# Performance work log

Hardware: AMD Instinct MI355X
Metric: run time of the kernel (lower is better)

Reference implementation:

```python
import jax, jax.numpy as jnp
import numpy as np

N, NUM_CLASSES, FEAT_DIM = 32768, 395, 512


def setup_inputs() -> dict:
    key = jax.random.key(0)
    k1, k2, k3, k4 = jax.random.split(key, 4)
    modal1_inputs = jax.random.normal(k1, (N, FEAT_DIM), dtype=jnp.float32)
    modal2_inputs = jax.random.normal(k2, (N, FEAT_DIM), dtype=jnp.float32)
    targets = jax.random.randint(k3, (N,), 0, NUM_CLASSES)
    # learned centers parameter: torch.rand -> uniform [0, 1)
    centers = jax.random.uniform(k4, (NUM_CLASSES, FEAT_DIM), dtype=jnp.float32)
    return {
        "modal1_inputs": modal1_inputs,
        "modal2_inputs": modal2_inputs,
        "centers": centers,
        "targets": targets,
    }


def _smooth_l1(a, b):
    # SmoothL1Loss with default beta=1.0, reduction='mean'
    d = jnp.abs(a - b)
    return jnp.mean(jnp.where(d < 1.0, 0.5 * d * d, d - 0.5))


def reference(modal1_inputs, modal2_inputs, centers, targets):
    num_classes = centers.shape[0]
    # Per-label mean (the original O(N^2) loop is exactly a segment mean
    # gathered back per sample).
    ones = jnp.ones((targets.shape[0],), dtype=modal1_inputs.dtype)
    counts = jax.ops.segment_sum(ones, targets, num_segments=num_classes)
    counts = jnp.maximum(counts, 1.0)  # empty classes never gathered
    sum1 = jax.ops.segment_sum(modal1_inputs, targets, num_segments=num_classes)
    sum2 = jax.ops.segment_sum(modal2_inputs, targets, num_segments=num_classes)
    centersR = (sum1 / counts[:, None])[targets]  # [N, D]
    centersT = (sum2 / counts[:, None])[targets]  # [N, D]
    gathered_centers = centers[targets]           # [N, D]
    loss = _smooth_l1(centersR, gathered_centers) + _smooth_l1(centersT, gathered_centers)
    return loss
```

## Files before the change

### kernel.cpp

```cpp
#include <hip/hip_runtime.h>

#define NS 32768
#define NC 395
#define FD 512
#define SPL 8
#define CHUNK (NS / SPL)
#define TPB 256
#define NEL (NC * FD)

__device__ float g_partial[SPL * 2 * NC * FD];
__device__ int   g_pcount[SPL * NC];

__device__ __forceinline__ void f4add(float4& a, const float4 b) {
    a.x += b.x; a.y += b.y; a.z += b.z; a.w += b.w;
}

__global__ __launch_bounds__(TPB)
void gather_sum_kernel(const float4* __restrict__ m1,
                       const float4* __restrict__ m2,
                       const int* __restrict__ targets,
                       float* __restrict__ out) {
    int c   = blockIdx.x >> 3;
    int s   = blockIdx.x & (SPL - 1);
    int tid = threadIdx.x;

    if (blockIdx.x == 0 && tid == 0) out[0] = 0.0f;

    __shared__ int sidx[CHUNK];
    __shared__ int scnt;
    __shared__ float4 cmb[2][128];

    int sbase = s * CHUNK;
    const int4* t4 = reinterpret_cast<const int4*>(targets + sbase);
    int4 ta = t4[tid];
    int4 tb = t4[tid + TPB];
    int4 tc = t4[tid + 2 * TPB];
    int4 td = t4[tid + 3 * TPB];
    if (tid == 0) scnt = 0;
    __syncthreads();
    int i0 = sbase + 4 * tid;
    int i1 = sbase + 4 * (tid + TPB);
    int i2 = sbase + 4 * (tid + 2 * TPB);
    int i3 = sbase + 4 * (tid + 3 * TPB);
    if (ta.x == c) sidx[atomicAdd(&scnt, 1)] = i0;
    if (ta.y == c) sidx[atomicAdd(&scnt, 1)] = i0 + 1;
    if (ta.z == c) sidx[atomicAdd(&scnt, 1)] = i0 + 2;
    if (ta.w == c) sidx[atomicAdd(&scnt, 1)] = i0 + 3;
    if (tb.x == c) sidx[atomicAdd(&scnt, 1)] = i1;
    if (tb.y == c) sidx[atomicAdd(&scnt, 1)] = i1 + 1;
    if (tb.z == c) sidx[atomicAdd(&scnt, 1)] = i1 + 2;
    if (tb.w == c) sidx[atomicAdd(&scnt, 1)] = i1 + 3;
    if (tc.x == c) sidx[atomicAdd(&scnt, 1)] = i2;
    if (tc.y == c) sidx[atomicAdd(&scnt, 1)] = i2 + 1;
    if (tc.z == c) sidx[atomicAdd(&scnt, 1)] = i2 + 2;
    if (tc.w == c) sidx[atomicAdd(&scnt, 1)] = i2 + 3;
    if (td.x == c) sidx[atomicAdd(&scnt, 1)] = i3;
    if (td.y == c) sidx[atomicAdd(&scnt, 1)] = i3 + 1;
    if (td.z == c) sidx[atomicAdd(&scnt, 1)] = i3 + 2;
    if (td.w == c) sidx[atomicAdd(&scnt, 1)] = i3 + 3;
    __syncthreads();
    int cnt = scnt;

    int wid  = tid >> 6;
    int mod  = wid >> 1;
    int wsub = wid & 1;
    int lane = tid & 63;
    const float4* src = mod ? m2 : m1;

    float4 z = make_float4(0.f, 0.f, 0.f, 0.f);
    float4 aA0 = z, aB0 = z, aA1 = z, aB1 = z;

    int j = wsub;
    for (; j + 6 < cnt; j += 8) {
        const float4* p0 = src + (size_t)sidx[j]     * 128;
        const float4* p1 = src + (size_t)sidx[j + 2] * 128;
        const float4* p2 = src + (size_t)sidx[j + 4] * 128;
        const float4* p3 = src + (size_t)sidx[j + 6] * 128;
        float4 vA0 = p0[lane], vB0 = p0[lane + 64];
        float4 vA1 = p1[lane], vB1 = p1[lane + 64];
        float4 vA2 = p2[lane], vB2 = p2[lane + 64];
        float4 vA3 = p3[lane], vB3 = p3[lane + 64];
        f4add(aA0, vA0); f4add(aB0, vB0);
        f4add(aA1, vA1); f4add(aB1, vB1);
        f4add(aA0, vA2); f4add(aB0, vB2);
        f4add(aA1, vA3); f4add(aB1, vB3);
    }
    for (; j < cnt; j += 2) {
        const float4* p = src + (size_t)sidx[j] * 128;
        f4add(aA0, p[lane]); f4add(aB0, p[lane + 64]);
    }
    f4add(aA0, aA1); f4add(aB0, aB1);

    if (wsub == 0) {
        cmb[mod][lane]      = aA0;
        cmb[mod][lane + 64] = aB0;
    }
    __syncthreads();
    if (wsub == 1) {
        float4 rA = cmb[mod][lane];      f4add(rA, aA0);
        float4 rB = cmb[mod][lane + 64]; f4add(rB, aB0);
        float4* dst = reinterpret_cast<float4*>(g_partial);
        size_t base = (((size_t)s * 2 + mod) * NC + c) * 128;
        dst[base + lane]      = rA;
        dst[base + lane + 64] = rB;
    }
    if (tid == 0) g_pcount[s * NC + c] = cnt;
}

__device__ __forceinline__ float smooth_l1(float d) {
    d = fabsf(d);
    return d < 1.0f ? 0.5f * d * d : d - 0.5f;
}

__global__ void loss_kernel(const float* __restrict__ centers,
                            float* __restrict__ out) {
    __shared__ float scnt[NC];
    int t = threadIdx.x;
    for (int c = t; c < NC; c += 256) {
        int sc = 0;
        #pragma unroll
        for (int k = 0; k < SPL; k++) sc += g_pcount[k * NC + c];
        scnt[c] = (float)sc;
    }
    __syncthreads();

    float val = 0.0f;
    for (int gid = blockIdx.x * 256 + t; gid < NEL; gid += gridDim.x * 256) {
        int c = gid >> 9;
        float cnt = scnt[c];
        if (cnt > 0.0f) {
            float s1 = 0.0f, s2 = 0.0f;
            #pragma unroll
            for (int k = 0; k < SPL; k++) {
                s1 += g_partial[(size_t)(2 * k)     * NEL + gid];
                s2 += g_partial[(size_t)(2 * k + 1) * NEL + gid];
            }
            float ctr = centers[gid];
            float inv = 1.0f / cnt;
            val += cnt * (smooth_l1(s1 * inv - ctr) + smooth_l1(s2 * inv - ctr));
        }
    }

    for (int off = 32; off > 0; off >>= 1)
        val += __shfl_down(val, off, 64);
    __shared__ float wsum[4];
    int lane = t & 63, wid = t >> 6;
    if (lane == 0) wsum[wid] = val;
    __syncthreads();
    if (t == 0) {
        float sm = wsum[0] + wsum[1] + wsum[2] + wsum[3];
        atomicAdd(out, sm * 5.9604644775390625e-08f);
    }
}

extern "C" void kernel_launch(void* const* d_in, const int* in_sizes, int n_in,
                              void* d_out, int out_size, void* d_ws, size_t ws_size,
                              hipStream_t stream) {
    const float4* m1 = (const float4*)d_in[0];
    const float4* m2 = (const float4*)d_in[1];
    const float* centers = (const float*)d_in[2];
    const int* targets = (const int*)d_in[3];
    float* out = (float*)d_out;

    gather_sum_kernel<<<NC * SPL, TPB, 0, stream>>>(m1, m2, targets, out);
    loss_kernel<<<512, 256, 0, stream>>>(centers, out);
}
```

Baseline: 168.5 us.

## Replace per-block target scanning with global counting sort of sample indices

Before, every one of the class×split blocks re-read its whole chunk of the targets array and filtered it with shared-memory atomics. Now a histogram, a prefix scan and a scatter kernel build a sorted index list once. Each class's range in that list is split into 4 quarters per gather block, which replaces the 8 chunk splits. This removes the redundant target scanning and halves the partial buffer the loss kernel reads, at the cost of three extra small launches including a single-block prefix kernel.

```diff
diff --git a/kernel.cpp b/kernel.cpp
--- a/kernel.cpp
+++ b/kernel.cpp
@@ -3,79 +3,99 @@
 #define NS 32768
 #define NC 395
 #define FD 512
-#define SPL 8
-#define CHUNK (NS / SPL)
-#define TPB 256
 #define NEL (NC * FD)
 
-__device__ float g_partial[SPL * 2 * NC * FD];
-__device__ int   g_pcount[SPL * NC];
+#define HBLK 64
+#define QPC 4
+
+__device__ int   g_histp[HBLK * NC];
+__device__ int   g_off[NC + 1];
+__device__ int   g_cur[NC];
+__device__ int   g_sorted[NS];
+__device__ float g_part[QPC * 2 * NC * FD];
+
+__global__ __launch_bounds__(256)
+void k_hist(const int* __restrict__ targets) {
+    __shared__ int h[NC];
+    int t = threadIdx.x;
+    for (int c = t; c < NC; c += 256) h[c] = 0;
+    __syncthreads();
+    int base = blockIdx.x * 512;
+    atomicAdd(&h[targets[base + t]], 1);
+    atomicAdd(&h[targets[base + t + 256]], 1);
+    __syncthreads();
+    for (int c = t; c < NC; c += 256) g_histp[blockIdx.x * NC + c] = h[c];
+}
+
+__global__ __launch_bounds__(512)
+void k_prefix(float* __restrict__ out) {
+    __shared__ int sh[512];
+    int t = threadIdx.x;
+    int v = 0;
+    if (t < NC)
+        for (int b = 0; b < HBLK; b++) v += g_histp[b * NC + t];
+    sh[t] = v;
+    __syncthreads();
+    for (int off = 1; off < 512; off <<= 1) {
+        int x = sh[t];
+        if (t >= off) x += sh[t - off];
+        __syncthreads();
+        sh[t] = x;
+        __syncthreads();
+    }
+    if (t < NC) {
+        int excl = sh[t] - v;
+        g_off[t] = excl;
+        g_cur[t] = excl;
+    }
+    if (t == NC - 1) g_off[NC] = sh[t];
+    if (t == 0) out[0] = 0.0f;
+}
+
+__global__ __launch_bounds__(256)
+void k_scatter(const int* __restrict__ targets) {
+    int i = blockIdx.x * 256 + threadIdx.x;
+    int c = targets[i];
+    int pos = atomicAdd(&g_cur[c], 1);
+    g_sorted[pos] = i;
+}
 
 __device__ __forceinline__ void f4add(float4& a, const float4 b) {
     a.x += b.x; a.y += b.y; a.z += b.z; a.w += b.w;
 }
 
-__global__ __launch_bounds__(TPB)
-void gather_sum_kernel(const float4* __restrict__ m1,
-                       const float4* __restrict__ m2,
-                       const int* __restrict__ targets,
-                       float* __restrict__ out) {
-    int c   = blockIdx.x >> 3;
-    int s   = blockIdx.x & (SPL - 1);
+__global__ __launch_bounds__(256)
+void k_gather(const float4* __restrict__ m1, const float4* __restrict__ m2) {
+    int c   = blockIdx.x >> 2;
+    int q   = blockIdx.x & (QPC - 1);
     int tid = threadIdx.x;
 
-    if (blockIdx.x == 0 && tid == 0) out[0] = 0.0f;
-
-    __shared__ int sidx[CHUNK];
-    __shared__ int scnt;
-    __shared__ float4 cmb[2][128];
-
-    int sbase = s * CHUNK;
-    const int4* t4 = reinterpret_cast<const int4*>(targets + sbase);
-    int4 ta = t4[tid];
-    int4 tb = t4[tid + TPB];
-    int4 tc = t4[tid + 2 * TPB];
-    int4 td = t4[tid + 3 * TPB];
-    if (tid == 0) scnt = 0;
-    __syncthreads();
-    int i0 = sbase + 4 * tid;
-    int i1 = sbase + 4 * (tid + TPB);
-    int i2 = sbase + 4 * (tid + 2 * TPB);
-    int i3 = sbase + 4 * (tid + 3 * TPB);
-    if (ta.x == c) sidx[atomicAdd(&scnt, 1)] = i0;
-    if (ta.y == c) sidx[atomicAdd(&scnt, 1)] = i0 + 1;
-    if (ta.z == c) sidx[atomicAdd(&scnt, 1)] = i0 + 2;
-    if (ta.w == c) sidx[atomicAdd(&scnt, 1)] = i0 + 3;
-    if (tb.x == c) sidx[atomicAdd(&scnt, 1)] = i1;
-    if (tb.y == c) sidx[atomicAdd(&scnt, 1)] = i1 + 1;
-    if (tb.z == c) sidx[atomicAdd(&scnt, 1)] = i1 + 2;
-    if (tb.w == c) sidx[atomicAdd(&scnt, 1)] = i1 + 3;
-    if (tc.x == c) sidx[atomicAdd(&scnt, 1)] = i2;
-    if (tc.y == c) sidx[atomicAdd(&scnt, 1)] = i2 + 1;
-    if (tc.z == c) sidx[atomicAdd(&scnt, 1)] = i2 + 2;
-    if (tc.w == c) sidx[atomicAdd(&scnt, 1)] = i2 + 3;
-    if (td.x == c) sidx[atomicAdd(&scnt, 1)] = i3;
-    if (td.y == c) sidx[atomicAdd(&scnt, 1)] = i3 + 1;
-    if (td.z == c) sidx[atomicAdd(&scnt, 1)] = i3 + 2;
-    if (td.w == c) sidx[atomicAdd(&scnt, 1)] = i3 + 3;
-    __syncthreads();
-    int cnt = scnt;
+    int o0 = g_off[c], o1 = g_off[c + 1];
+    int n  = o1 - o0;
+    int s0 = o0 + ((n * q) >> 2);
+    int s1 = o0 + ((n * (q + 1)) >> 2);
 
     int wid  = tid >> 6;
     int mod  = wid >> 1;
-    int wsub = wid & 1;
+    int par  = wid & 1;
     int lane = tid & 63;
     const float4* src = mod ? m2 : m1;
 
     float4 z = make_float4(0.f, 0.f, 0.f, 0.f);
     float4 aA0 = z, aB0 = z, aA1 = z, aB1 = z;
 
-    int j = wsub;
-    for (; j + 6 < cnt; j += 8) {
-        const float4* p0 = src + (size_t)sidx[j]     * 128;
-        const float4* p1 = src + (size_t)sidx[j + 2] * 128;
-        const float4* p2 = src + (size_t)sidx[j + 4] * 128;
-        const float4* p3 = src + (size_t)sidx[j + 6] * 128;
+    __shared__ float4 cmb[2][128];
+
+    int j = s0 + par;
+    for (; j + 6 < s1; j += 8) {
+        int i0 = g_sorted[j];
+        int i1 = g_sorted[j + 2];
+        int i2 = g_sorted[j + 4];
+        int i3 = g_sorted[j + 6];
+        const float4* p0 = src + (size_t)i0 * 128;
+        const float4* p1 = src + (size_t)i1 * 128;
+        const float4* p2 = src + (size_t)i2 * 128;
+        const float4* p3 = src + (size_t)i3 * 128;
         float4 vA0 = p0[lane], vB0 = p0[lane + 64];
         float4 vA1 = p1[lane], vB1 = p1[lane + 64];
         float4 vA2 = p2[lane], vB2 = p2[lane + 64];
@@ -85,26 +105,25 @@
         f4add(aA0, vA2); f4add(aB0, vB2);
         f4add(aA1, vA3); f4add(aB1, vB3);
     }
-    for (; j < cnt; j += 2) {
-        const float4* p = src + (size_t)sidx[j] * 128;
+    for (; j < s1; j += 2) {
+        const float4* p = src + (size_t)g_sorted[j] * 128;
         f4add(aA0, p[lane]); f4add(aB0, p[lane + 64]);
     }
     f4add(aA0, aA1); f4add(aB0, aB1);
 
-    if (wsub == 0) {
+    if (par == 0) {
         cmb[mod][lane]      = aA0;
         cmb[mod][lane + 64] = aB0;
     }
     __syncthreads();
-    if (wsub == 1) {
+    if (par == 1) {
         float4 rA = cmb[mod][lane];      f4add(rA, aA0);
         float4 rB = cmb[mod][lane + 64]; f4add(rB, aB0);
-        float4* dst = reinterpret_cast<float4*>(g_partial);
-        size_t base = (((size_t)s * 2 + mod) * NC + c) * 128;
+        float4* dst = reinterpret_cast<float4*>(g_part);
+        size_t base = (((size_t)q * 2 + mod) * NC + c) * 128;
         dst[base + lane]      = rA;
         dst[base + lane + 64] = rB;
     }
-    if (tid == 0) g_pcount[s * NC + c] = cnt;
 }
 
 __device__ __forceinline__ float smooth_l1(float d) {
@@ -112,16 +131,12 @@
     return d < 1.0f ? 0.5f * d * d : d - 0.5f;
 }
 
-__global__ void loss_kernel(const float* __restrict__ centers,
-                            float* __restrict__ out) {
+__global__ void k_loss(const float* __restrict__ centers,
+                       float* __restrict__ out) {
     __shared__ float scnt[NC];
     int t = threadIdx.x;
-    for (int c = t; c < NC; c += 256) {
-        int sc = 0;
-        #pragma unroll
-        for (int k = 0; k < SPL; k++) sc += g_pcount[k * NC + c];
-        scnt[c] = (float)sc;
-    }
+    for (int c = t; c < NC; c += 256)
+        scnt[c] = (float)(g_off[c + 1] - g_off[c]);
     __syncthreads();
 
     float val = 0.0f;
@@ -131,9 +146,9 @@
         if (cnt > 0.0f) {
             float s1 = 0.0f, s2 = 0.0f;
             #pragma unroll
-            for (int k = 0; k < SPL; k++) {
-                s1 += g_partial[(size_t)(2 * k)     * NEL + gid];
-                s2 += g_partial[(size_t)(2 * k + 1) * NEL + gid];
+            for (int k = 0; k < QPC; k++) {
+                s1 += g_part[(size_t)(2 * k)     * NEL + gid];
+                s2 += g_part[(size_t)(2 * k + 1) * NEL + gid];
             }
             float ctr = centers[gid];
             float inv = 1.0f / cnt;
@@ -162,6 +177,9 @@
     const int* targets = (const int*)d_in[3];
     float* out = (float*)d_out;
 
-    gather_sum_kernel<<<NC * SPL, TPB, 0, stream>>>(m1, m2, targets, out);
-    loss_kernel<<<512, 256, 0, stream>>>(centers, out);
+    k_hist<<<NS / 512, 256, 0, stream>>>(targets);
+    k_prefix<<<1, 512, 0, stream>>>(out);
+    k_scatter<<<NS / 256, 256, 0, stream>>>(targets);
+    k_gather<<<NC * QPC, 256, 0, stream>>>(m1, m2);
+    k_loss<<<512, 256, 0, stream>>>(centers, out);
 }
```

Result: slower. 184.3 us (+9.3%).

## Replace per-class gather with streaming row pass and shared-memory atomic accumulation

Applied to the files above, without the earlier changes.

The segment sum is restructured. Each block used to scan the targets for one class and gather matching rows. Now each block streams a contiguous row range for one 32-float column slice and accumulates into a per-class table in LDS with shared atomics. Inputs are read once, fully coalesced, with prefetching, which removes the repeated target scans and scattered row gathers. The cost is heavy LDS atomic traffic, only 512 blocks, and a larger partial buffer (16 splits) that the loss kernel must now reduce, which it does with float4 loads.

```diff
diff --git a/kernel.cpp b/kernel.cpp
--- a/kernel.cpp
+++ b/kernel.cpp
@@ -3,108 +3,102 @@
 #define NS 32768
 #define NC 395
 #define FD 512
-#define SPL 8
-#define CHUNK (NS / SPL)
-#define TPB 256
 #define NEL (NC * FD)
 
-__device__ float g_partial[SPL * 2 * NC * FD];
-__device__ int   g_pcount[SPL * NC];
+#define RS 16
+#define CT 16
+#define TF4 8
+#define ROWS_PB (NS / RS)
+#define ASTRIDE 33
+
+__device__ float g_part[2 * RS * NC * FD];
+__device__ int   g_hist[RS * NC];
 
 __device__ __forceinline__ void f4add(float4& a, const float4 b) {
     a.x += b.x; a.y += b.y; a.z += b.z; a.w += b.w;
 }
 
-__global__ __launch_bounds__(TPB)
-void gather_sum_kernel(const float4* __restrict__ m1,
-                       const float4* __restrict__ m2,
-                       const int* __restrict__ targets,
-                       float* __restrict__ out) {
-    int c   = blockIdx.x >> 3;
-    int s   = blockIdx.x & (SPL - 1);
-    int tid = threadIdx.x;
+__global__ __launch_bounds__(256, 2)
+void k_stream(const float4* __restrict__ m1, const float4* __restrict__ m2,
+              const int* __restrict__ targets, float* __restrict__ out) {
+    int bid = blockIdx.x;
+    int ct  = bid & (CT - 1);
+    int mod = (bid >> 4) & 1;
+    int rs  = bid >> 5;
+    int t   = threadIdx.x;
 
-    if (blockIdx.x == 0 && tid == 0) out[0] = 0.0f;
+    __shared__ float acc[NC * ASTRIDE];
+    __shared__ int   tg[ROWS_PB];
 
-    __shared__ int sidx[CHUNK];
-    __shared__ int scnt;
-    __shared__ float4 cmb[2][128];
+    for (int i = t; i < NC * ASTRIDE; i += 256) acc[i] = 0.f;
 
-    int sbase = s * CHUNK;
-    const int4* t4 = reinterpret_cast<const int4*>(targets + sbase);
-    int4 ta = t4[tid];
-    int4 tb = t4[tid + TPB];
-    int4 tc = t4[tid + 2 * TPB];
-    int4 td = t4[tid + 3 * TPB];
-    if (tid == 0) scnt = 0;
+    const int4* t4 = reinterpret_cast<const int4*>(targets + rs * ROWS_PB);
+    reinterpret_cast<int4*>(tg)[t]       = t4[t];
+    reinterpret_cast<int4*>(tg)[t + 256] = t4[t + 256];
+    if (bid == 0 && t == 0) out[0] = 0.f;
     __syncthreads();
-    int i0 = sbase + 4 * tid;
-    int i1 = sbase + 4 * (tid + TPB);
-    int i2 = sbase + 4 * (tid + 2 * TPB);
-    int i3 = sbase + 4 * (tid + 3 * TPB);
-    if (ta.x == c) sidx[atomicAdd(&scnt, 1)] = i0;
-    if (ta.y == c) sidx[atomicAdd(&scnt, 1)] = i0 + 1;
-    if (ta.z == c) sidx[atomicAdd(&scnt, 1)] = i0 + 2;
-    if (ta.w == c) sidx[atomicAdd(&scnt, 1)] = i0 + 3;
-    if (tb.x == c) sidx[atomicAdd(&scnt, 1)] = i1;
-    if (tb.y == c) sidx[atomicAdd(&scnt, 1)] = i1 + 1;
-    if (tb.z == c) sidx[atomicAdd(&scnt, 1)] = i1 + 2;
-    if (tb.w == c) sidx[atomicAdd(&scnt, 1)] = i1 + 3;
-    if (tc.x == c) sidx[atomicAdd(&scnt, 1)] = i2;
-    if (tc.y == c) sidx[atomicAdd(&scnt, 1)] = i2 + 1;
-    if (tc.z == c) sidx[atomicAdd(&scnt, 1)] = i2 + 2;
-    if (tc.w == c) sidx[atomicAdd(&scnt, 1)] = i2 + 3;
-    if (td.x == c) sidx[atomicAdd(&scnt, 1)] = i3;
-    if (td.y == c) sidx[atomicAdd(&scnt, 1)] = i3 + 1;
-    if (td.z == c) sidx[atomicAdd(&scnt, 1)] = i3 + 2;
-    if (td.w == c) sidx[atomicAdd(&scnt, 1)] = i3 + 3;
+
+    const float4* src = mod ? m2 : m1;
+    int rsub = t >> 3;
+    int cf4  = t & 7;
+    const float4* sp = src + (size_t)rs * ROWS_PB * 128 + ct * TF4 + cf4;
+
+    float4 v0,v1,v2,v3,v4,v5,v6,v7;
+    v0 = sp[(size_t)(0*32 + rsub) * 128];
+    v1 = sp[(size_t)(1*32 + rsub) * 128];
+    v2 = sp[(size_t)(2*32 + rsub) * 128];
+    v3 = sp[(size_t)(3*32 + rsub) * 128];
+    v4 = sp[(size_t)(4*32 + rsub) * 128];
+    v5 = sp[(size_t)(5*32 + rsub) * 128];
+    v6 = sp[(size_t)(6*32 + rsub) * 128];
+    v7 = sp[(size_t)(7*32 + rsub) * 128];
+
+    #define ACCUM(U, V)                                                      \
+    {   int cls = tg[(rb + U) * 32 + rsub];                                  \
+        float* ap = &acc[cls * ASTRIDE + cf4 * 4];                           \
+        atomicAdd(ap + 0, V.x); atomicAdd(ap + 1, V.y);                      \
+        atomicAdd(ap + 2, V.z); atomicAdd(ap + 3, V.w); }
+
+    for (int rb = 0; rb < 56; rb += 8) {
+        float4 w0,w1,w2,w3,w4,w5,w6,w7;
+        w0 = sp[(size_t)((rb+ 8)*32 + rsub) * 128];
+        w1 = sp[(size_t)((rb+ 9)*32 + rsub) * 128];
+        w2 = sp[(size_t)((rb+10)*32 + rsub) * 128];
+        w3 = sp[(size_t)((rb+11)*32 + rsub) * 128];
+        w4 = sp[(size_t)((rb+12)*32 + rsub) * 128];
+        w5 = sp[(size_t)((rb+13)*32 + rsub) * 128];
+        w6 = sp[(size_t)((rb+14)*32 + rsub) * 128];
+        w7 = sp[(size_t)((rb+15)*32 + rsub) * 128];
+        ACCUM(0, v0) ACCUM(1, v1) ACCUM(2, v2) ACCUM(3, v3)
+        ACCUM(4, v4) ACCUM(5, v5) ACCUM(6, v6) ACCUM(7, v7)
+        v0=w0; v1=w1; v2=w2; v3=w3; v4=w4; v5=w5; v6=w6; v7=w7;
+    }
+    {
+        const int rb = 56;
+        ACCUM(0, v0) ACCUM(1, v1) ACCUM(2, v2) ACCUM(3, v3)
+        ACCUM(4, v4) ACCUM(5, v5) ACCUM(6, v6) ACCUM(7, v7)
+    }
+    #undef ACCUM
     __syncthreads();
-    int cnt = scnt;
 
-    int wid  = tid >> 6;
-    int mod  = wid >> 1;
-    int wsub = wid & 1;
-    int lane = tid & 63;
-    const float4* src = mod ? m2 : m1;
+    float4* dst = reinterpret_cast<float4*>(g_part)
+                + (size_t)(mod * RS + rs) * (NEL / 4) + ct * TF4;
+    for (int i = t; i < NC * TF4; i += 256) {
+        int cls = i >> 3, cf = i & 7;
+        const float* ap = &acc[cls * ASTRIDE + cf * 4];
+        float4 vv; vv.x = ap[0]; vv.y = ap[1]; vv.z = ap[2]; vv.w = ap[3];
+        dst[(size_t)cls * (FD / 4) + cf] = vv;
+    }
 
-    float4 z = make_float4(0.f, 0.f, 0.f, 0.f);
-    float4 aA0 = z, aB0 = z, aA1 = z, aB1 = z;
-
-    int j = wsub;
-    for (; j + 6 < cnt; j += 8) {
-        const float4* p0 = src + (size_t)sidx[j]     * 128;
-        const float4* p1 = src + (size_t)sidx[j + 2] * 128;
-        const float4* p2 = src + (size_t)sidx[j + 4] * 128;
-        const float4* p3 = src + (size_t)sidx[j + 6] * 128;
-        float4 vA0 = p0[lane], vB0 = p0[lane + 64];
-        float4 vA1 = p1[lane], vB1 = p1[lane + 64];
-        float4 vA2 = p2[lane], vB2 = p2[lane + 64];
-        float4 vA3 = p3[lane], vB3 = p3[lane + 64];
-        f4add(aA0, vA0); f4add(aB0, vB0);
-        f4add(aA1, vA1); f4add(aB1, vB1);
-        f4add(aA0, vA2); f4add(aB0, vB2);
-        f4add(aA1, vA3); f4add(aB1, vB3);
+    if (ct == 0 && mod == 0) {
+        __syncthreads();
+        int* h = reinterpret_cast<int*>(acc);
+        for (int i = t; i < NC; i += 256) h[i] = 0;
+        __syncthreads();
+        for (int i = t; i < ROWS_PB; i += 256) atomicAdd(&h[tg[i]], 1);
+        __syncthreads();
+        for (int i = t; i < NC; i += 256) g_hist[rs * NC + i] = h[i];
     }
-    for (; j < cnt; j += 2) {
-        const float4* p = src + (size_t)sidx[j] * 128;
-        f4add(aA0, p[lane]); f4add(aB0, p[lane + 64]);
-    }
-    f4add(aA0, aA1); f4add(aB0, aB1);
-
-    if (wsub == 0) {
-        cmb[mod][lane]      = aA0;
-        cmb[mod][lane + 64] = aB0;
-    }
-    __syncthreads();
-    if (wsub == 1) {
-        float4 rA = cmb[mod][lane];      f4add(rA, aA0);
-        float4 rB = cmb[mod][lane + 64]; f4add(rB, aB0);
-        float4* dst = reinterpret_cast<float4*>(g_partial);
-        size_t base = (((size_t)s * 2 + mod) * NC + c) * 128;
-        dst[base + lane]      = rA;
-        dst[base + lane + 64] = rB;
-    }
-    if (tid == 0) g_pcount[s * NC + c] = cnt;
 }
 
 __device__ __forceinline__ float smooth_l1(float d) {
@@ -112,32 +106,38 @@
     return d < 1.0f ? 0.5f * d * d : d - 0.5f;
 }
 
-__global__ void loss_kernel(const float* __restrict__ centers,
-                            float* __restrict__ out) {
+__global__ __launch_bounds__(256)
+void k_loss(const float* __restrict__ centers, float* __restrict__ out) {
     __shared__ float scnt[NC];
     int t = threadIdx.x;
     for (int c = t; c < NC; c += 256) {
-        int sc = 0;
+        int s = 0;
         #pragma unroll
-        for (int k = 0; k < SPL; k++) sc += g_pcount[k * NC + c];
-        scnt[c] = (float)sc;
+        for (int k = 0; k < RS; ++k) s += g_hist[k * NC + c];
+        scnt[c] = (float)s;
     }
     __syncthreads();
 
-    float val = 0.0f;
-    for (int gid = blockIdx.x * 256 + t; gid < NEL; gid += gridDim.x * 256) {
-        int c = gid >> 9;
-        float cnt = scnt[c];
-        if (cnt > 0.0f) {
-            float s1 = 0.0f, s2 = 0.0f;
+    const float4* ctr4  = reinterpret_cast<const float4*>(centers);
+    const float4* part4 = reinterpret_cast<const float4*>(g_part);
+    const int NE4 = NEL / 4;
+    float val = 0.f;
+    for (int g = blockIdx.x * 256 + t; g < NE4; g += gridDim.x * 256) {
+        int cls = g >> 7;
+        float cnt = scnt[cls];
+        if (cnt > 0.f) {
+            float4 s1 = make_float4(0,0,0,0), s2 = make_float4(0,0,0,0);
             #pragma unroll
-            for (int k = 0; k < SPL; k++) {
-                s1 += g_partial[(size_t)(2 * k)     * NEL + gid];
-                s2 += g_partial[(size_t)(2 * k + 1) * NEL + gid];
+            for (int k = 0; k < RS; ++k) {
+                f4add(s1, part4[(size_t)k        * NE4 + g]);
+                f4add(s2, part4[(size_t)(RS + k) * NE4 + g]);
             }
-            float ctr = centers[gid];
-            float inv = 1.0f / cnt;
-            val += cnt * (smooth_l1(s1 * inv - ctr) + smooth_l1(s2 * inv - ctr));
+            float4 c4 = ctr4[g];
+            float inv = 1.f / cnt;
+            val += cnt * (smooth_l1(s1.x * inv - c4.x) + smooth_l1(s2.x * inv - c4.x)
+                        + smooth_l1(s1.y * inv - c4.y) + smooth_l1(s2.y * inv - c4.y)
+                        + smooth_l1(s1.z * inv - c4.z) + smooth_l1(s2.z * inv - c4.z)
+                        + smooth_l1(s1.w * inv - c4.w) + smooth_l1(s2.w * inv - c4.w));
         }
     }
 
@@ -162,6 +162,6 @@
     const int* targets = (const int*)d_in[3];
     float* out = (float*)d_out;
 
-    gather_sum_kernel<<<NC * SPL, TPB, 0, stream>>>(m1, m2, targets, out);
-    loss_kernel<<<512, 256, 0, stream>>>(centers, out);
+    k_stream<<<RS * 2 * CT, 256, 0, stream>>>(m1, m2, targets, out);
+    k_loss<<<200, 256, 0, stream>>>(centers, out);
 }
```

Result: slower. 292.2 us (+73.4%).

## Split gather into two halves per class and vectorize loss reduction

Applied to the files above, without the earlier changes.

Reduces the per-class split from 8 chunks to 2, so each block scans 16K targets and accumulates more rows, with a 2048-entry shared index cap. The loss kernel now reads only two partial sums and uses float4 loads, shrinking the partial buffer traffic. The gather loop unroll rises to 6 rows per iteration with three accumulator pairs. The trade-off is far fewer blocks (790 instead of 3160), which lowers parallelism for the memory-bound gather, and each block spends longer on its target scan.

```diff
diff --git a/kernel.cpp b/kernel.cpp
--- a/kernel.cpp
+++ b/kernel.cpp
@@ -3,108 +3,108 @@
 #define NS 32768
 #define NC 395
 #define FD 512
-#define SPL 8
-#define CHUNK (NS / SPL)
-#define TPB 256
 #define NEL (NC * FD)
+#define HALF (NS / 2)
+#define SCAP 2048
 
-__device__ float g_partial[SPL * 2 * NC * FD];
-__device__ int   g_pcount[SPL * NC];
+__device__ float g_sum[2 * 2 * NC * FD];
+__device__ int   g_cnt[2 * NC];
 
 __device__ __forceinline__ void f4add(float4& a, const float4 b) {
     a.x += b.x; a.y += b.y; a.z += b.z; a.w += b.w;
 }
 
-__global__ __launch_bounds__(TPB)
-void gather_sum_kernel(const float4* __restrict__ m1,
-                       const float4* __restrict__ m2,
-                       const int* __restrict__ targets,
-                       float* __restrict__ out) {
-    int c   = blockIdx.x >> 3;
-    int s   = blockIdx.x & (SPL - 1);
-    int tid = threadIdx.x;
+__global__ __launch_bounds__(256)
+void k_gather(const float4* __restrict__ m1, const float4* __restrict__ m2,
+              const int* __restrict__ targets, float* __restrict__ out)
+{
+    const int c   = blockIdx.x >> 1;
+    const int h   = blockIdx.x & 1;
+    const int tid = threadIdx.x;
 
     if (blockIdx.x == 0 && tid == 0) out[0] = 0.0f;
 
-    __shared__ int sidx[CHUNK];
+    __shared__ int sidx[SCAP];
     __shared__ int scnt;
     __shared__ float4 cmb[2][128];
 
-    int sbase = s * CHUNK;
-    const int4* t4 = reinterpret_cast<const int4*>(targets + sbase);
-    int4 ta = t4[tid];
-    int4 tb = t4[tid + TPB];
-    int4 tc = t4[tid + 2 * TPB];
-    int4 td = t4[tid + 3 * TPB];
+    const int4* t4 = reinterpret_cast<const int4*>(targets + h * HALF);
+    int4 a0 = t4[tid          ], a1 = t4[tid +  1 * 256],
+         a2 = t4[tid + 2 * 256], a3 = t4[tid +  3 * 256],
+         a4 = t4[tid + 4 * 256], a5 = t4[tid +  5 * 256],
+         a6 = t4[tid + 6 * 256], a7 = t4[tid +  7 * 256];
     if (tid == 0) scnt = 0;
     __syncthreads();
-    int i0 = sbase + 4 * tid;
-    int i1 = sbase + 4 * (tid + TPB);
-    int i2 = sbase + 4 * (tid + 2 * TPB);
-    int i3 = sbase + 4 * (tid + 3 * TPB);
-    if (ta.x == c) sidx[atomicAdd(&scnt, 1)] = i0;
-    if (ta.y == c) sidx[atomicAdd(&scnt, 1)] = i0 + 1;
-    if (ta.z == c) sidx[atomicAdd(&scnt, 1)] = i0 + 2;
-    if (ta.w == c) sidx[atomicAdd(&scnt, 1)] = i0 + 3;
-    if (tb.x == c) sidx[atomicAdd(&scnt, 1)] = i1;
-    if (tb.y == c) sidx[atomicAdd(&scnt, 1)] = i1 + 1;
-    if (tb.z == c) sidx[atomicAdd(&scnt, 1)] = i1 + 2;
-    if (tb.w == c) sidx[atomicAdd(&scnt, 1)] = i1 + 3;
-    if (tc.x == c) sidx[atomicAdd(&scnt, 1)] = i2;
-    if (tc.y == c) sidx[atomicAdd(&scnt, 1)] = i2 + 1;
-    if (tc.z == c) sidx[atomicAdd(&scnt, 1)] = i2 + 2;
-    if (tc.w == c) sidx[atomicAdd(&scnt, 1)] = i2 + 3;
-    if (td.x == c) sidx[atomicAdd(&scnt, 1)] = i3;
-    if (td.y == c) sidx[atomicAdd(&scnt, 1)] = i3 + 1;
-    if (td.z == c) sidx[atomicAdd(&scnt, 1)] = i3 + 2;
-    if (td.w == c) sidx[atomicAdd(&scnt, 1)] = i3 + 3;
+    int4 b0 = t4[tid +  8 * 256], b1 = t4[tid +  9 * 256],
+         b2 = t4[tid + 10 * 256], b3 = t4[tid + 11 * 256],
+         b4 = t4[tid + 12 * 256], b5 = t4[tid + 13 * 256],
+         b6 = t4[tid + 14 * 256], b7 = t4[tid + 15 * 256];
+
+#define CHK(V, K)                                                           \
+    {   int ib = h * HALF + 4 * (tid + (K) * 256);                          \
+        if (V.x == c) { int p = atomicAdd(&scnt, 1); if (p < SCAP) sidx[p] = ib;     } \
+        if (V.y == c) { int p = atomicAdd(&scnt, 1); if (p < SCAP) sidx[p] = ib + 1; } \
+        if (V.z == c) { int p = atomicAdd(&scnt, 1); if (p < SCAP) sidx[p] = ib + 2; } \
+        if (V.w == c) { int p = atomicAdd(&scnt, 1); if (p < SCAP) sidx[p] = ib + 3; } }
+    CHK(a0, 0) CHK(a1, 1) CHK(a2, 2)  CHK(a3, 3)
+    CHK(a4, 4) CHK(a5, 5) CHK(a6, 6)  CHK(a7, 7)
+    CHK(b0, 8) CHK(b1, 9) CHK(b2, 10) CHK(b3, 11)
+    CHK(b4,12) CHK(b5,13) CHK(b6, 14) CHK(b7, 15)
+#undef CHK
     __syncthreads();
-    int cnt = scnt;
+    int cnt = scnt; if (cnt > SCAP) cnt = SCAP;
 
-    int wid  = tid >> 6;
-    int mod  = wid >> 1;
-    int wsub = wid & 1;
-    int lane = tid & 63;
+    const int wid  = tid >> 6;
+    const int mod  = wid >> 1;
+    const int par  = wid & 1;
+    const int lane = tid & 63;
     const float4* src = mod ? m2 : m1;
 
     float4 z = make_float4(0.f, 0.f, 0.f, 0.f);
-    float4 aA0 = z, aB0 = z, aA1 = z, aB1 = z;
+    float4 aA0 = z, aB0 = z, aA1 = z, aB1 = z, aA2 = z, aB2 = z;
 
-    int j = wsub;
-    for (; j + 6 < cnt; j += 8) {
-        const float4* p0 = src + (size_t)sidx[j]     * 128;
-        const float4* p1 = src + (size_t)sidx[j + 2] * 128;
-        const float4* p2 = src + (size_t)sidx[j + 4] * 128;
-        const float4* p3 = src + (size_t)sidx[j + 6] * 128;
+    int j = par;
+    for (; j + 10 < cnt; j += 12) {
+        const float4* p0 = src + (size_t)sidx[j]      * 128;
+        const float4* p1 = src + (size_t)sidx[j +  2] * 128;
+        const float4* p2 = src + (size_t)sidx[j +  4] * 128;
+        const float4* p3 = src + (size_t)sidx[j +  6] * 128;
+        const float4* p4 = src + (size_t)sidx[j +  8] * 128;
+        const float4* p5 = src + (size_t)sidx[j + 10] * 128;
         float4 vA0 = p0[lane], vB0 = p0[lane + 64];
         float4 vA1 = p1[lane], vB1 = p1[lane + 64];
         float4 vA2 = p2[lane], vB2 = p2[lane + 64];
         float4 vA3 = p3[lane], vB3 = p3[lane + 64];
+        float4 vA4 = p4[lane], vB4 = p4[lane + 64];
+        float4 vA5 = p5[lane], vB5 = p5[lane + 64];
         f4add(aA0, vA0); f4add(aB0, vB0);
         f4add(aA1, vA1); f4add(aB1, vB1);
-        f4add(aA0, vA2); f4add(aB0, vB2);
-        f4add(aA1, vA3); f4add(aB1, vB3);
+        f4add(aA2, vA2); f4add(aB2, vB2);
+        f4add(aA0, vA3); f4add(aB0, vB3);
+        f4add(aA1, vA4); f4add(aB1, vB4);
+        f4add(aA2, vA5); f4add(aB2, vB5);
     }
     for (; j < cnt; j += 2) {
         const float4* p = src + (size_t)sidx[j] * 128;
         f4add(aA0, p[lane]); f4add(aB0, p[lane + 64]);
     }
     f4add(aA0, aA1); f4add(aB0, aB1);
+    f4add(aA0, aA2); f4add(aB0, aB2);
 
-    if (wsub == 0) {
+    if (par == 0) {
         cmb[mod][lane]      = aA0;
         cmb[mod][lane + 64] = aB0;
     }
     __syncthreads();
-    if (wsub == 1) {
+    if (par == 1) {
         float4 rA = cmb[mod][lane];      f4add(rA, aA0);
         float4 rB = cmb[mod][lane + 64]; f4add(rB, aB0);
-        float4* dst = reinterpret_cast<float4*>(g_partial);
-        size_t base = (((size_t)s * 2 + mod) * NC + c) * 128;
-        dst[base + lane]      = rA;
-        dst[base + lane + 64] = rB;
+        float4* dst = reinterpret_cast<float4*>(g_sum)
+                    + (size_t)((h * 2 + mod) * NC + c) * 128;
+        dst[lane]      = rA;
+        dst[lane + 64] = rB;
     }
-    if (tid == 0) g_pcount[s * NC + c] = cnt;
+    if (tid == 0) g_cnt[h * NC + c] = cnt;
 }
 
 __device__ __forceinline__ float smooth_l1(float d) {
@@ -112,32 +112,30 @@
     return d < 1.0f ? 0.5f * d * d : d - 0.5f;
 }
 
-__global__ void loss_kernel(const float* __restrict__ centers,
-                            float* __restrict__ out) {
+__global__ __launch_bounds__(256)
+void k_loss(const float* __restrict__ centers, float* __restrict__ out) {
     __shared__ float scnt[NC];
     int t = threadIdx.x;
-    for (int c = t; c < NC; c += 256) {
-        int sc = 0;
-        #pragma unroll
-        for (int k = 0; k < SPL; k++) sc += g_pcount[k * NC + c];
-        scnt[c] = (float)sc;
-    }
+    for (int c = t; c < NC; c += 256)
+        scnt[c] = (float)(g_cnt[c] + g_cnt[NC + c]);
     __syncthreads();
 
-    float val = 0.0f;
-    for (int gid = blockIdx.x * 256 + t; gid < NEL; gid += gridDim.x * 256) {
-        int c = gid >> 9;
-        float cnt = scnt[c];
-        if (cnt > 0.0f) {
-            float s1 = 0.0f, s2 = 0.0f;
-            #pragma unroll
-            for (int k = 0; k < SPL; k++) {
-                s1 += g_partial[(size_t)(2 * k)     * NEL + gid];
-                s2 += g_partial[(size_t)(2 * k + 1) * NEL + gid];
-            }
-            float ctr = centers[gid];
-            float inv = 1.0f / cnt;
-            val += cnt * (smooth_l1(s1 * inv - ctr) + smooth_l1(s2 * inv - ctr));
+    const float4* ctr4 = reinterpret_cast<const float4*>(centers);
+    const float4* s4   = reinterpret_cast<const float4*>(g_sum);
+    const int NE4 = NEL / 4;
+    float val = 0.f;
+    for (int g = blockIdx.x * 256 + t; g < NE4; g += gridDim.x * 256) {
+        int cls = g >> 7;
+        float cnt = scnt[cls];
+        if (cnt > 0.f) {
+            float4 s1 = s4[g];              f4add(s1, s4[2 * NE4 + g]);
+            float4 s2 = s4[NE4 + g];        f4add(s2, s4[3 * NE4 + g]);
+            float4 c4 = ctr4[g];
+            float inv = 1.f / cnt;
+            val += cnt * (smooth_l1(s1.x * inv - c4.x) + smooth_l1(s2.x * inv - c4.x)
+                        + smooth_l1(s1.y * inv - c4.y) + smooth_l1(s2.y * inv - c4.y)
+                        + smooth_l1(s1.z * inv - c4.z) + smooth_l1(s2.z * inv - c4.z)
+                        + smooth_l1(s1.w * inv - c4.w) + smooth_l1(s2.w * inv - c4.w));
         }
     }
 
@@ -162,6 +160,6 @@
     const int* targets = (const int*)d_in[3];
     float* out = (float*)d_out;
 
-    gather_sum_kernel<<<NC * SPL, TPB, 0, stream>>>(m1, m2, targets, out);
-    loss_kernel<<<512, 256, 0, stream>>>(centers, out);
+    k_gather<<<NC * 2, 256, 0, stream>>>(m1, m2, targets, out);
+    k_loss<<<200, 256, 0, stream>>>(centers, out);
 }
```

After: 164.9 us. -2.2%, faster.
